# Kernel tuning notes

Measured on AMD Instinct MI355X. Metric: run time of the kernel, lower is better.

The kernel has to match this reference:

```python
import jax, jax.numpy as jnp
import numpy as np

NUM_ITEMS = 100000
D_SEM = 768
D_PROMPT = 384
D_MODEL = 2048
B, T = 64, 200


def setup_inputs() -> dict:
    key = jax.random.key(0)
    k_ids, k_len, k_sem, k_vp, k_w = jax.random.split(key, 5)
    ids = jax.random.randint(k_ids, (B, T), 0, NUM_ITEMS, dtype=jnp.int64 if jax.config.jax_enable_x64 else jnp.int32)
    lengths = jax.random.randint(k_len, (B,), 1, T + 1, dtype=ids.dtype)
    # positions beyond each sequence length are padding (-1), as produced by the dataloader
    pos = jnp.arange(T, dtype=ids.dtype)[None, :]
    ids = jnp.where(pos < lengths[:, None], ids, -1)
    E_sem = jax.random.normal(k_sem, (NUM_ITEMS, D_SEM), dtype=jnp.float32)
    v_prompt = 0.02 * jax.random.normal(k_vp, (NUM_ITEMS, D_PROMPT), dtype=jnp.float32)
    # nn.Linear weight: [out_features, in_features]
    proj_w = jax.random.normal(k_w, (D_MODEL, D_SEM + D_PROMPT), dtype=jnp.float32) * (1.0 / np.sqrt(D_SEM + D_PROMPT))
    return {"batch_item_ids_padded": ids, "batch_lengths": lengths,
            "E_sem": E_sem, "v_prompt": v_prompt, "proj_w": proj_w}


def reference(batch_item_ids_padded, batch_lengths, E_sem, v_prompt, proj_w):
    """Vectorized build_inputs_embeds: gather + concat + projection, masked.
    Returns (embeds [B,T,d_model], amask [B,T], tok_item_ids [B,T])."""
    ids = batch_item_ids_padded
    num_items = E_sem.shape[0]
    valid = (ids >= 0) & (ids < num_items)            # [B,T]
    safe = jnp.where(valid, ids, 0)                   # clamp for safe gather
    sem = E_sem[safe]                                 # [B,T,d_sem]
    vp = v_prompt[safe]                               # [B,T,d_prompt]
    cat = jnp.concatenate([sem, vp], axis=-1)         # [B,T,d_sem+d_prompt]
    tok = jnp.einsum('btk,dk->btd', cat, proj_w)      # [B,T,d_model]
    embeds = jnp.where(valid[..., None], tok, jnp.zeros((), tok.dtype))
    amask = valid.astype(jnp.int32)
    tok_item_ids = jnp.where(valid, ids, -1)
    return embeds, amask, tok_item_ids
```

## Files before the change

kernel.cpp:

```cpp
#include <hip/hip_runtime.h>
#include <stdint.h>

constexpr int BB = 64, TT = 200;
constexpr int M  = BB * TT;
constexpr int DSEM = 768, DPR = 384;
constexpr int Kd = DSEM + DPR;
constexpr int Nd = 2048;
constexpr int NUM_ITEMS = 100000;
constexpr int BK = 64;

constexpr int GATHER_BLOCKS = (M * Kd / 4) / 256;
constexpr int WCONV_BLOCKS  = (Nd * Kd / 4) / 256;
constexpr int MASK_BLOCKS   = (M + 255) / 256;

typedef short bf16x8 __attribute__((ext_vector_type(8)));
typedef float f32x4  __attribute__((ext_vector_type(4)));

__device__ __forceinline__ unsigned short f2bf(float f) {
  union { float f; uint32_t u; } v; v.f = f;
  uint32_t u = v.u;
  u += 0x7fffu + ((u >> 16) & 1u);
  return (unsigned short)(u >> 16);
}

__global__ void prep_kernel(const int* __restrict__ ids,
                            const float* __restrict__ Esem,
                            const float* __restrict__ vpr,
                            const float* __restrict__ pw,
                            unsigned short* __restrict__ A,
                            unsigned short* __restrict__ Wb,
                            float* __restrict__ amask,
                            float* __restrict__ tok) {
  const int b = blockIdx.x;
  const int tid = threadIdx.x;
  if (b < GATHER_BLOCKS) {
    unsigned g = (unsigned)b * 256u + tid;
    unsigned row = g / 288u;
    unsigned col = (g - row * 288u) * 4u;
    int id = ids[row];
    bool valid = (id >= 0) && (id < NUM_ITEMS);
    int safe = valid ? id : 0;
    const float* src = (col < (unsigned)DSEM)
                         ? (Esem + (size_t)safe * DSEM + col)
                         : (vpr  + (size_t)safe * DPR  + (col - DSEM));
    float4 v = *(const float4*)src;
    if (!valid) { v.x = 0.f; v.y = 0.f; v.z = 0.f; v.w = 0.f; }
    ushort4 o;
    o.x = f2bf(v.x); o.y = f2bf(v.y); o.z = f2bf(v.z); o.w = f2bf(v.w);
    *(ushort4*)(A + (size_t)row * Kd + col) = o;
  } else if (b < GATHER_BLOCKS + WCONV_BLOCKS) {
    int g = (b - GATHER_BLOCKS) * 256 + tid;
    int e = g * 4;
    float4 v = *(const float4*)(pw + e);
    ushort4 o;
    o.x = f2bf(v.x); o.y = f2bf(v.y); o.z = f2bf(v.z); o.w = f2bf(v.w);
    *(ushort4*)(Wb + e) = o;
  } else {
    int i = (b - GATHER_BLOCKS - WCONV_BLOCKS) * 256 + tid;
    if (i < M) {
      int id = ids[i];
      bool valid = (id >= 0) && (id < NUM_ITEMS);
      amask[i] = valid ? 1.0f : 0.0f;
      tok[i]   = valid ? (float)id : -1.0f;
    }
  }
}

__device__ __forceinline__ void async16(const void* gsrc, void* ldst) {
  __builtin_amdgcn_global_load_lds(
      (const __attribute__((address_space(1))) unsigned int*)gsrc,
      (__attribute__((address_space(3))) unsigned int*)ldst,
      16, 0, 0);
}

__global__ __launch_bounds__(256) void gemm_kernel(const unsigned short* __restrict__ A,
                                                   const unsigned short* __restrict__ Wb,
                                                   float* __restrict__ C) {
  __shared__ unsigned short lds_a[128 * BK];
  __shared__ unsigned short lds_b[128 * BK];

  const int tid  = threadIdx.x;
  const int lane = tid & 63;
  const int wave = tid >> 6;
  const int wm = wave >> 1, wn = wave & 1;
  const int quad = lane >> 4, lm = lane & 15;
  const int m0 = blockIdx.x * 128;
  const int n0 = blockIdx.y * 128;

  const int srow   = tid >> 3;
  const int schunk = tid & 7;

  f32x4 acc[4][4];
#pragma unroll
  for (int i = 0; i < 4; ++i)
#pragma unroll
    for (int j = 0; j < 4; ++j) acc[i][j] = (f32x4){0.f, 0.f, 0.f, 0.f};

  for (int kt = 0; kt < Kd / BK; ++kt) {
    const int k0 = kt * BK;
#pragma unroll
    for (int r = 0; r < 4; ++r) {
      const int row = r * 32 + srow;
      const int gch = schunk ^ (row & 7);
      const unsigned short* ga = A + (size_t)(m0 + row) * Kd + k0 + gch * 8;
      async16(ga, lds_a + (size_t)(r * 256 + wave * 64) * 8);
      const unsigned short* gb = Wb + (size_t)(n0 + row) * Kd + k0 + gch * 8;
      async16(gb, lds_b + (size_t)(r * 256 + wave * 64) * 8);
    }
    __syncthreads();

#pragma unroll
    for (int h = 0; h < 2; ++h) {
      bf16x8 af[4], bfr[4];
#pragma unroll
      for (int mi = 0; mi < 4; ++mi) {
        const int row = wm * 64 + mi * 16 + lm;
        af[mi] = *(const bf16x8*)(lds_a + row * BK + ((h * 4 + quad) ^ (row & 7)) * 8);
      }
#pragma unroll
      for (int ni = 0; ni < 4; ++ni) {
        const int row = wn * 64 + ni * 16 + lm;
        bfr[ni] = *(const bf16x8*)(lds_b + row * BK + ((h * 4 + quad) ^ (row & 7)) * 8);
      }
#pragma unroll
      for (int mi = 0; mi < 4; ++mi)
#pragma unroll
        for (int ni = 0; ni < 4; ++ni)
          acc[mi][ni] = __builtin_amdgcn_mfma_f32_16x16x32_bf16(af[mi], bfr[ni], acc[mi][ni], 0, 0, 0);
    }
    __syncthreads();
  }

#pragma unroll
  for (int mi = 0; mi < 4; ++mi) {
#pragma unroll
    for (int ni = 0; ni < 4; ++ni) {
      const int row = m0 + wm * 64 + mi * 16 + quad * 4;
      const int col = n0 + wn * 64 + ni * 16 + lm;
#pragma unroll
      for (int i = 0; i < 4; ++i)
        C[(size_t)(row + i) * Nd + col] = acc[mi][ni][i];
    }
  }
}

extern "C" void kernel_launch(void* const* d_in, const int* in_sizes, int n_in,
                              void* d_out, int out_size, void* d_ws, size_t ws_size,
                              hipStream_t stream) {
  const int*   ids  = (const int*)d_in[0];
  const float* Esem = (const float*)d_in[2];
  const float* vpr  = (const float*)d_in[3];
  const float* pw   = (const float*)d_in[4];

  float* out_emb   = (float*)d_out;
  float* out_amask = out_emb + (size_t)M * Nd;
  float* out_tok   = out_amask + M;

  unsigned short* A  = (unsigned short*)d_ws;
  unsigned short* Wb = A + (size_t)M * Kd;

  prep_kernel<<<GATHER_BLOCKS + WCONV_BLOCKS + MASK_BLOCKS, 256, 0, stream>>>(
      ids, Esem, vpr, pw, A, Wb, out_amask, out_tok);
  gemm_kernel<<<dim3(M / 128, Nd / 128), 256, 0, stream>>>(A, Wb, out_emb);
}
```

Before: 526.3 us.

## Stage GEMM epilogue through LDS for float4 stores; widen prep to 8 elements

The GEMM epilogue now writes each wave's accumulator tile into the idle shared-memory A buffer, then reads it back so each lane issues float4 stores covering full contiguous row segments. Before, each lane wrote scalar floats in a scattered pattern, so output writes were poorly coalesced. The gather/convert prep kernel now has each thread handle 8 elements instead of 4, halving the block count. This adds LDS traffic in the epilogue and leaves an unused dummy helper in the code.

```diff
diff --git a/kernel.cpp b/kernel.cpp
--- a/kernel.cpp
+++ b/kernel.cpp
@@ -9,8 +9,8 @@
 constexpr int NUM_ITEMS = 100000;
 constexpr int BK = 64;
 
-constexpr int GATHER_BLOCKS = (M * Kd / 4) / 256;
-constexpr int WCONV_BLOCKS  = (Nd * Kd / 4) / 256;
+constexpr int GATHER_BLOCKS = (M * Kd / 8) / 256;
+constexpr int WCONV_BLOCKS  = (Nd * Kd / 8) / 256;
 constexpr int MASK_BLOCKS   = (M + 255) / 256;
 
 typedef short bf16x8 __attribute__((ext_vector_type(8)));
@@ -21,6 +21,10 @@
   uint32_t u = v.u;
   u += 0x7fffu + ((u >> 16) & 1u);
   return (unsigned short)(u >> 16);
+}
+
+__device__ __forceinline__ ushort4 cvt8(float4 a, float4 b2) {
+  ushort4 dummy; return dummy;
 }
 
 __global__ void prep_kernel(const int* __restrict__ ids,
@@ -35,26 +39,36 @@
   const int tid = threadIdx.x;
   if (b < GATHER_BLOCKS) {
     unsigned g = (unsigned)b * 256u + tid;
-    unsigned row = g / 288u;
-    unsigned col = (g - row * 288u) * 4u;
+    unsigned row = g / 144u;
+    unsigned col = (g - row * 144u) * 8u;
     int id = ids[row];
     bool valid = (id >= 0) && (id < NUM_ITEMS);
     int safe = valid ? id : 0;
     const float* src = (col < (unsigned)DSEM)
                          ? (Esem + (size_t)safe * DSEM + col)
                          : (vpr  + (size_t)safe * DPR  + (col - DSEM));
-    float4 v = *(const float4*)src;
-    if (!valid) { v.x = 0.f; v.y = 0.f; v.z = 0.f; v.w = 0.f; }
-    ushort4 o;
-    o.x = f2bf(v.x); o.y = f2bf(v.y); o.z = f2bf(v.z); o.w = f2bf(v.w);
-    *(ushort4*)(A + (size_t)row * Kd + col) = o;
+    float4 v0 = *(const float4*)src;
+    float4 v1 = *(const float4*)(src + 4);
+    if (!valid) {
+      v0.x = v0.y = v0.z = v0.w = 0.f;
+      v1.x = v1.y = v1.z = v1.w = 0.f;
+    }
+    ushort4 o0, o1;
+    o0.x = f2bf(v0.x); o0.y = f2bf(v0.y); o0.z = f2bf(v0.z); o0.w = f2bf(v0.w);
+    o1.x = f2bf(v1.x); o1.y = f2bf(v1.y); o1.z = f2bf(v1.z); o1.w = f2bf(v1.w);
+    unsigned short* dst = A + (size_t)row * Kd + col;
+    *(ushort4*)dst       = o0;
+    *(ushort4*)(dst + 4) = o1;
   } else if (b < GATHER_BLOCKS + WCONV_BLOCKS) {
     int g = (b - GATHER_BLOCKS) * 256 + tid;
-    int e = g * 4;
-    float4 v = *(const float4*)(pw + e);
-    ushort4 o;
-    o.x = f2bf(v.x); o.y = f2bf(v.y); o.z = f2bf(v.z); o.w = f2bf(v.w);
-    *(ushort4*)(Wb + e) = o;
+    int e = g * 8;
+    float4 v0 = *(const float4*)(pw + e);
+    float4 v1 = *(const float4*)(pw + e + 4);
+    ushort4 o0, o1;
+    o0.x = f2bf(v0.x); o0.y = f2bf(v0.y); o0.z = f2bf(v0.z); o0.w = f2bf(v0.w);
+    o1.x = f2bf(v1.x); o1.y = f2bf(v1.y); o1.z = f2bf(v1.z); o1.w = f2bf(v1.w);
+    *(ushort4*)(Wb + e)     = o0;
+    *(ushort4*)(Wb + e + 4) = o1;
   } else {
     int i = (b - GATHER_BLOCKS - WCONV_BLOCKS) * 256 + tid;
     if (i < M) {
@@ -76,8 +90,8 @@
 __global__ __launch_bounds__(256) void gemm_kernel(const unsigned short* __restrict__ A,
                                                    const unsigned short* __restrict__ Wb,
                                                    float* __restrict__ C) {
-  __shared__ unsigned short lds_a[128 * BK];
-  __shared__ unsigned short lds_b[128 * BK];
+  __shared__ __align__(16) unsigned short lds_a[128 * BK];
+  __shared__ __align__(16) unsigned short lds_b[128 * BK];
 
   const int tid  = threadIdx.x;
   const int lane = tid & 63;
@@ -131,15 +145,22 @@
     __syncthreads();
   }
 
+  float* lw = (float*)lds_a + wave * 1024;
+  const int r4  = lane >> 4;
+  const int c16 = lane & 15;
 #pragma unroll
   for (int mi = 0; mi < 4; ++mi) {
 #pragma unroll
-    for (int ni = 0; ni < 4; ++ni) {
-      const int row = m0 + wm * 64 + mi * 16 + quad * 4;
-      const int col = n0 + wn * 64 + ni * 16 + lm;
+    for (int ni = 0; ni < 4; ++ni)
 #pragma unroll
       for (int i = 0; i < 4; ++i)
-        C[(size_t)(row + i) * Nd + col] = acc[mi][ni][i];
+        lw[(quad * 4 + i) * 64 + ni * 16 + lm] = acc[mi][ni][i];
+#pragma unroll
+    for (int j = 0; j < 4; ++j) {
+      float4 v = *(const float4*)(lw + (j * 4 + r4) * 64 + c16 * 4);
+      const int row = m0 + wm * 64 + mi * 16 + j * 4 + r4;
+      const int col = n0 + wn * 64 + c16 * 4;
+      *(float4*)(C + (size_t)row * Nd + col) = v;
     }
   }
 }
```

Result: no change. 523.5 us (-0.5%).
